# Kernel optimization log

Measured on AMD Instinct MI355X. Metric: run time of the kernel, lower is better.

The kernel has to match this reference:

```python
import jax, jax.numpy as jnp
import numpy as np

D_MODEL = 1024
NHEADS = 16
D_K = D_MODEL // NHEADS


def setup_inputs() -> dict:
    key = jax.random.key(0)
    ks = jax.random.split(key, 12)
    B, S = 2, 2048
    scale = 1.0 / np.sqrt(D_MODEL)
    inp = {
        "query": jax.random.normal(ks[0], (B, S, D_MODEL), dtype=jnp.float32),
        "key": jax.random.normal(ks[1], (B, S, D_MODEL), dtype=jnp.float32),
        "value": jax.random.normal(ks[2], (B, S, D_MODEL), dtype=jnp.float32),
        "mask": jax.random.randint(ks[3], (B, 1, S, S), 0, 2, dtype=jnp.int32),
        "Wq": jax.random.normal(ks[4], (D_MODEL, D_MODEL), dtype=jnp.float32) * scale,
        "bq": jnp.zeros((D_MODEL,), dtype=jnp.float32),
        "Wk": jax.random.normal(ks[5], (D_MODEL, D_MODEL), dtype=jnp.float32) * scale,
        "bk": jnp.zeros((D_MODEL,), dtype=jnp.float32),
        "Wv": jax.random.normal(ks[6], (D_MODEL, D_MODEL), dtype=jnp.float32) * scale,
        "bv": jnp.zeros((D_MODEL,), dtype=jnp.float32),
        "Wo": jax.random.normal(ks[7], (D_MODEL, D_MODEL), dtype=jnp.float32) * scale,
        "bo": jnp.zeros((D_MODEL,), dtype=jnp.float32),
    }
    return inp


def _split_heads(x):
    # [B, S, (H*D)] -> [B, H, S, D]
    B, S, _ = x.shape
    return x.reshape(B, S, NHEADS, D_K).transpose(0, 2, 1, 3)


def reference(query, key, value, mask, Wq, bq, Wk, bk, Wv, bv, Wo, bo):
    B, Sq, _ = query.shape
    q = _split_heads(query @ Wq + bq)            # [B, H, Sq, Dk]
    k = _split_heads(key @ Wk + bk)              # [B, H, Sk, Dk]
    v = _split_heads(value @ Wv + bv)            # [B, H, Sk, Dk]
    # scores: [B, H, Sq, Sk], scaled by sqrt(d_k)
    scores = jnp.einsum("bhqd,bhkd->bhqk", q, k) / np.sqrt(D_K).astype(np.float32)
    scores = jnp.where(mask == 0, jnp.float32(-1e12), scores)
    weights = jax.nn.softmax(scores, axis=-1)
    out = jnp.einsum("bhqk,bhkd->bhqd", weights, v)  # [B, H, Sq, Dk]
    out = out.transpose(0, 2, 1, 3).reshape(B, Sq, D_MODEL)
    return out @ Wo + bo  # dropout is identity in eval / p=0
```

## Files before the change

kernel.cpp:

```cpp
#include <hip/hip_runtime.h>
#include <math.h>

#define D_MODEL 1024
#define NHEADS  16
#define DK      64
#define BATCH   2
#define SEQ     2048
#define M_TOTAL (BATCH * SEQ)
#define NT      (SEQ / 64)
#define CK1 0.18033688011112042f
#define CK0 -17.312340490667561f

typedef __attribute__((ext_vector_type(8))) short bf16x8;
typedef __attribute__((ext_vector_type(4))) float f32x4;

__device__ __forceinline__ unsigned short f2bf(float f) {
    union { float f; unsigned int i; } v; v.f = f;
    return (unsigned short)((v.i + 0x7FFFu + ((v.i >> 16) & 1u)) >> 16);
}

__device__ __forceinline__ void async_copy16(const void* g, void* l) {
    __builtin_amdgcn_global_load_lds(
        (const __attribute__((address_space(1))) unsigned int*)g,
        (__attribute__((address_space(3))) unsigned int*)l, 16, 0, 0);
}

struct Cvt3 { const float* s[3]; unsigned short* d[3]; };
__global__ __launch_bounds__(256)
void cvt_flat(const Cvt3 a)
{
    const float* __restrict__ s = a.s[blockIdx.z];
    unsigned short* __restrict__ d = a.d[blockIdx.z];
    const size_t i = ((size_t)blockIdx.x * 256 + threadIdx.x) * 4;
    const float4 v = *reinterpret_cast<const float4*>(&s[i]);
    ushort4 o;
    o.x = f2bf(v.x); o.y = f2bf(v.y); o.z = f2bf(v.z); o.w = f2bf(v.w);
    *reinterpret_cast<ushort4*>(&d[i]) = o;
}

struct Cvt4 { const float* s[4]; unsigned short* d[4]; };
__global__ __launch_bounds__(256)
void cvt_wt(const Cvt4 a)
{
    __shared__ unsigned short t[32][33];
    const float* __restrict__ W = a.s[blockIdx.z];
    unsigned short* __restrict__ WT = a.d[blockIdx.z];
    const int tx = threadIdx.x & 31;
    const int ty = threadIdx.x >> 5;
    const int nb = blockIdx.x << 5;
    const int kb = blockIdx.y << 5;
#pragma unroll
    for (int i = 0; i < 4; ++i)
        t[ty + (i << 3)][tx] = f2bf(W[(size_t)(kb + ty + (i << 3)) * D_MODEL + nb + tx]);
    __syncthreads();
#pragma unroll
    for (int i = 0; i < 4; ++i)
        WT[(size_t)(nb + ty + (i << 3)) * D_MODEL + kb + tx] = t[tx][ty + (i << 3)];
}

__global__ __launch_bounds__(256)
void mask_pack(const int* __restrict__ mask, unsigned long long* __restrict__ wm)
{
    const int tid  = threadIdx.x;
    const int lane = tid & 63;
    const int l15  = lane & 15;
    const int kg   = lane >> 4;
    const int wv   = ((int)blockIdx.x << 2) + (tid >> 6);
    const int t    = wv & 31;
    const int qw   = (wv >> 5) & 127;
    const int bb   = wv >> 12;

    const int* mb = mask + (size_t)bb * SEQ * SEQ;
    const int qrow = (qw << 4) + (kg << 2);
    const int kcol = (t << 6) + l15;
    unsigned long long* wout = wm + ((((size_t)bb * 128 + qw) * 32 + t) << 4);

#pragma unroll
    for (int r = 0; r < 4; ++r)
#pragma unroll
        for (int n = 0; n < 4; ++n) {
            const int m = mb[(size_t)(qrow + r) * SEQ + kcol + (n << 4)];
            const unsigned long long bal = __ballot(m != 0);
            if (lane == 0) wout[(r << 2) | n] = bal;
        }
}

template <typename OutT> struct GArgs {
    const unsigned short* X[3];
    const unsigned short* W[3];
    const float*          Bi[3];
    OutT*                 O[3];
};

__device__ __forceinline__ void st_out(float* p, float v) { *p = v; }
__device__ __forceinline__ void st_out(unsigned short* p, float v) { *p = f2bf(v); }

template <typename OutT>
__global__ __launch_bounds__(256)
void gemm_bf16(const GArgs<OutT> args, const int head_split)
{
    __shared__ __align__(16) unsigned short As[128][32];
    __shared__ __align__(16) unsigned short Bs[128][32];

    const unsigned short* __restrict__ X  = args.X[blockIdx.z];
    const unsigned short* __restrict__ WT = args.W[blockIdx.z];
    const float* __restrict__ bias        = args.Bi[blockIdx.z];
    OutT* __restrict__ out                = args.O[blockIdx.z];

    const int tid = threadIdx.x;
    const int wid = tid >> 6;
    const int wy  = wid >> 1;
    const int wx  = wid & 1;
    const int l15 = tid & 15;
    const int kg  = (tid >> 4) & 3;

    const int id = ((int)blockIdx.y << 3) | (int)blockIdx.x;
    const int sw = ((id & 7) << 5) | (id >> 3);
    const int n0 = (sw & 7) << 7;
    const int m0 = (sw >> 3) << 7;

    const int lane = tid & 63;
    const int gr   = lane >> 2;
    const int gc   = (lane & 3) << 3;
    const int c0   = wid << 1;

    f32x4 acc[4][4];
#pragma unroll
    for (int i = 0; i < 4; ++i)
#pragma unroll
        for (int j = 0; j < 4; ++j)
            acc[i][j] = (f32x4){0.f, 0.f, 0.f, 0.f};

#pragma unroll 1
    for (int t = 0; t < D_MODEL / 32; ++t) {
        const int k0 = t << 5;

        __syncthreads();
#pragma unroll
        for (int cc = 0; cc < 2; ++cc) {
            const int c = c0 + cc;
            async_copy16(&X[(size_t)(m0 + (c << 4) + gr) * D_MODEL + k0 + gc],
                         &As[c << 4][0]);
            async_copy16(&WT[(size_t)(n0 + (c << 4) + gr) * D_MODEL + k0 + gc],
                         &Bs[c << 4][0]);
        }
        __syncthreads();

        bf16x8 a[4], b[4];
#pragma unroll
        for (int i = 0; i < 4; ++i)
            a[i] = *reinterpret_cast<const bf16x8*>(
                &As[(wy << 6) + (i << 4) + l15][kg << 3]);
#pragma unroll
        for (int j = 0; j < 4; ++j)
            b[j] = *reinterpret_cast<const bf16x8*>(
                &Bs[(wx << 6) + (j << 4) + l15][kg << 3]);
#pragma unroll
        for (int i = 0; i < 4; ++i)
#pragma unroll
            for (int j = 0; j < 4; ++j)
                acc[i][j] = __builtin_amdgcn_mfma_f32_16x16x32_bf16(
                    a[i], b[j], acc[i][j], 0, 0, 0);
    }

    float bv[4];
#pragma unroll
    for (int j = 0; j < 4; ++j)
        bv[j] = bias[n0 + (wx << 6) + (j << 4) + l15];

#pragma unroll
    for (int i = 0; i < 4; ++i) {
#pragma unroll
        for (int r = 0; r < 4; ++r) {
            const int m = m0 + (wy << 6) + (i << 4) + (kg << 2) + r;
#pragma unroll
            for (int j = 0; j < 4; ++j) {
                const int n = n0 + (wx << 6) + (j << 4) + l15;
                const float val = acc[i][j][r] + bv[j];
                if (head_split) {
                    const int bbx = m >> 11;
                    const int ss  = m & (SEQ - 1);
                    const int hhx = n >> 6;
                    const int dd  = n & (DK - 1);
                    st_out(&out[((size_t)(bbx * NHEADS + hhx) * SEQ + ss) * DK + dd], val);
                } else {
                    st_out(&out[(size_t)m * D_MODEL + n], val);
                }
            }
        }
    }
}

__global__ __launch_bounds__(256)
void flash_mfma(const unsigned short* __restrict__ Qb,
                const unsigned short* __restrict__ Kb,
                const unsigned short* __restrict__ Vb,
                const unsigned long long* __restrict__ wmask,
                unsigned short* __restrict__ ctx)
{
    __shared__ __align__(16) unsigned short Kbf[64][72];
    __shared__ __align__(16) unsigned short Vt [64][72];
    __shared__ __align__(16) unsigned short Pq [4][16][72];

    const int tid  = threadIdx.x;
    const int w    = tid >> 6;
    const int lane = tid & 63;
    const int l15  = lane & 15;
    const int kg   = lane >> 4;

    const int bb = blockIdx.z;
    const int hh = blockIdx.y;
    const int q0 = blockIdx.x << 6;

    const unsigned short* Qh = Qb + (size_t)(bb * NHEADS + hh) * SEQ * DK;
    const unsigned short* Kh = Kb + (size_t)(bb * NHEADS + hh) * SEQ * DK;
    const unsigned short* Vh = Vb + (size_t)(bb * NHEADS + hh) * SEQ * DK;

    bf16x8 aq[2];
    {
        const unsigned short* qrow = Qh + (size_t)(q0 + w * 16 + l15) * DK + (kg << 3);
        aq[0] = *reinterpret_cast<const bf16x8*>(qrow);
        aq[1] = *reinterpret_cast<const bf16x8*>(qrow + 32);
    }

    const int krow = tid >> 2;
    const int kcb  = (tid & 3) << 4;
    const int vkb  = (tid & 15) << 2;
    const int vdb  = (tid >> 4) << 2;

    const int wbase = __builtin_amdgcn_readfirstlane(
        (bb * 128 + (q0 >> 4) + w) << 9);

    float l_lane[4] = {0.f, 0.f, 0.f, 0.f};
    f32x4 O4[4];
#pragma unroll
    for (int n = 0; n < 4; ++n) O4[n] = (f32x4){0.f, 0.f, 0.f, 0.f};

    uint4 kv0 = *reinterpret_cast<const uint4*>(Kh + (size_t)krow * DK + kcb);
    uint4 kv1 = *reinterpret_cast<const uint4*>(Kh + (size_t)krow * DK + kcb + 8);
    uint2 vr[4];
#pragma unroll
    for (int i = 0; i < 4; ++i)
        vr[i] = *reinterpret_cast<const uint2*>(Vh + (size_t)(vkb + i) * DK + vdb);

#pragma unroll 1
    for (int t = 0; t < NT; ++t) {
        __syncthreads();
        *reinterpret_cast<uint4*>(&Kbf[krow][kcb])     = kv0;
        *reinterpret_cast<uint4*>(&Kbf[krow][kcb + 8]) = kv1;
        {
            uint2 o;
            o.x = (vr[0].x & 0xFFFFu) | (vr[1].x << 16);
            o.y = (vr[2].x & 0xFFFFu) | (vr[3].x << 16);
            *reinterpret_cast<uint2*>(&Vt[vdb + 0][vkb]) = o;
            o.x = (vr[0].x >> 16) | (vr[1].x & 0xFFFF0000u);
            o.y = (vr[2].x >> 16) | (vr[3].x & 0xFFFF0000u);
            *reinterpret_cast<uint2*>(&Vt[vdb + 1][vkb]) = o;
            o.x = (vr[0].y & 0xFFFFu) | (vr[1].y << 16);
            o.y = (vr[2].y & 0xFFFFu) | (vr[3].y << 16);
            *reinterpret_cast<uint2*>(&Vt[vdb + 2][vkb]) = o;
            o.x = (vr[0].y >> 16) | (vr[1].y & 0xFFFF0000u);
            o.y = (vr[2].y >> 16) | (vr[3].y & 0xFFFF0000u);
            *reinterpret_cast<uint2*>(&Vt[vdb + 3][vkb]) = o;
        }
        __syncthreads();

        if (t + 1 < NT) {
            const int kn = (t + 1) << 6;
            kv0 = *reinterpret_cast<const uint4*>(Kh + (size_t)(kn + krow) * DK + kcb);
            kv1 = *reinterpret_cast<const uint4*>(Kh + (size_t)(kn + krow) * DK + kcb + 8);
#pragma unroll
            for (int i = 0; i < 4; ++i)
                vr[i] = *reinterpret_cast<const uint2*>(
                    Vh + (size_t)(kn + vkb + i) * DK + vdb);
        }

        const unsigned long long* wmt = wmask + wbase + (t << 4);
        unsigned long long wmv[16];
#pragma unroll
        for (int rn = 0; rn < 16; ++rn) wmv[rn] = wmt[rn];

        f32x4 S[4];
#pragma unroll
        for (int n = 0; n < 4; ++n) {
            const bf16x8 b0 = *reinterpret_cast<const bf16x8*>(
                &Kbf[16 * n + l15][kg << 3]);
            const bf16x8 b1 = *reinterpret_cast<const bf16x8*>(
                &Kbf[16 * n + l15][(kg << 3) + 32]);
            f32x4 acc = (f32x4){0.f, 0.f, 0.f, 0.f};
            acc = __builtin_amdgcn_mfma_f32_16x16x32_bf16(aq[0], b0, acc, 0, 0, 0);
            acc = __builtin_amdgcn_mfma_f32_16x16x32_bf16(aq[1], b1, acc, 0, 0, 0);
            S[n] = acc;
        }

#pragma unroll
        for (int n = 0; n < 4; ++n)
#pragma unroll
            for (int r = 0; r < 4; ++r) {
                float x = fmaf(S[n][r], CK1, CK0);
                __asm__("v_exp_f32 %0, %1" : "=v"(x) : "v"(x));
                __asm__("v_cndmask_b32 %0, 0, %1, %2"
                        : "=v"(x) : "v"(x), "s"(wmv[(r << 2) | n]));
                l_lane[r] += x;
                unsigned pk;
                __asm__("v_cvt_pk_bf16_f32 %0, %1, %2"
                        : "=v"(pk) : "v"(x), "v"(x));
                Pq[w][(kg << 2) + r][16 * n + l15] = (unsigned short)pk;
            }

        __asm__ volatile("s_waitcnt lgkmcnt(0)" ::: "memory");

        const bf16x8 ap0 = *reinterpret_cast<const bf16x8*>(&Pq[w][l15][kg << 3]);
        const bf16x8 ap1 = *reinterpret_cast<const bf16x8*>(&Pq[w][l15][(kg << 3) + 32]);
#pragma unroll
        for (int n = 0; n < 4; ++n) {
            const bf16x8 b0 = *reinterpret_cast<const bf16x8*>(
                &Vt[16 * n + l15][kg << 3]);
            const bf16x8 b1 = *reinterpret_cast<const bf16x8*>(
                &Vt[16 * n + l15][(kg << 3) + 32]);
            O4[n] = __builtin_amdgcn_mfma_f32_16x16x32_bf16(ap0, b0, O4[n], 0, 0, 0);
            O4[n] = __builtin_amdgcn_mfma_f32_16x16x32_bf16(ap1, b1, O4[n], 0, 0, 0);
        }
    }

#pragma unroll
    for (int r = 0; r < 4; ++r) {
        float rsum = l_lane[r];
        rsum += __shfl_xor(rsum, 1);
        rsum += __shfl_xor(rsum, 2);
        rsum += __shfl_xor(rsum, 4);
        rsum += __shfl_xor(rsum, 8);
        const float inv = 1.f / rsum;
        const size_t base =
            (size_t)(bb * SEQ + q0 + w * 16 + (kg << 2) + r) * D_MODEL + hh * DK + l15;
#pragma unroll
        for (int n = 0; n < 4; ++n)
            ctx[base + 16 * n] = f2bf(O4[n][r] * inv);
    }
}

extern "C" void kernel_launch(void* const* d_in, const int* in_sizes, int n_in,
                              void* d_out, int out_size, void* d_ws, size_t ws_size,
                              hipStream_t stream)
{
    const float* query = (const float*)d_in[0];
    const float* key   = (const float*)d_in[1];
    const float* value = (const float*)d_in[2];
    const int*   mask  = (const int*)d_in[3];
    const float* Wq = (const float*)d_in[4];
    const float* bq = (const float*)d_in[5];
    const float* Wk = (const float*)d_in[6];
    const float* bk = (const float*)d_in[7];
    const float* Wv = (const float*)d_in[8];
    const float* bv = (const float*)d_in[9];
    const float* Wo = (const float*)d_in[10];
    const float* bo = (const float*)d_in[11];

    unsigned short* ws = (unsigned short*)d_ws;
    const size_t TE = (size_t)M_TOTAL * D_MODEL;
    const size_t WE = (size_t)D_MODEL * D_MODEL;
    unsigned short* Xq  = ws;
    unsigned short* Xk  = Xq + TE;
    unsigned short* Xv  = Xk + TE;
    unsigned short* WTq = Xv + TE;
    unsigned short* WTk = WTq + WE;
    unsigned short* WTv = WTk + WE;
    unsigned short* WTo = WTv + WE;
    unsigned short* Qb  = WTo + WE;
    unsigned short* Kb  = Qb + TE;
    unsigned short* Vb  = Kb + TE;
    unsigned short* Ctx = Vb + TE;
    unsigned long long* WM = (unsigned long long*)(Ctx + TE);

    Cvt3 c3;
    c3.s[0] = query; c3.s[1] = key; c3.s[2] = value;
    c3.d[0] = Xq;    c3.d[1] = Xk;  c3.d[2] = Xv;
    cvt_flat<<<dim3(TE / 1024, 1, 3), 256, 0, stream>>>(c3);

    Cvt4 c4;
    c4.s[0] = Wq;  c4.s[1] = Wk;  c4.s[2] = Wv;  c4.s[3] = Wo;
    c4.d[0] = WTq; c4.d[1] = WTk; c4.d[2] = WTv; c4.d[3] = WTo;
    cvt_wt<<<dim3(32, 32, 4), 256, 0, stream>>>(c4);

    mask_pack<<<dim3(2048, 1, 1), 256, 0, stream>>>(mask, WM);

    GArgs<unsigned short> qkv;
    qkv.X[0] = Xq;  qkv.X[1] = Xk;  qkv.X[2] = Xv;
    qkv.W[0] = WTq; qkv.W[1] = WTk; qkv.W[2] = WTv;
    qkv.Bi[0] = bq; qkv.Bi[1] = bk; qkv.Bi[2] = bv;
    qkv.O[0] = Qb;  qkv.O[1] = Kb;  qkv.O[2] = Vb;
    gemm_bf16<unsigned short><<<dim3(8, 32, 3), 256, 0, stream>>>(qkv, 1);

    flash_mfma<<<dim3(SEQ / 64, NHEADS, BATCH), 256, 0, stream>>>(
        Qb, Kb, Vb, WM, Ctx);

    GArgs<float> op;
    op.X[0] = Ctx;  op.X[1] = Ctx;  op.X[2] = Ctx;
    op.W[0] = WTo;  op.W[1] = WTo;  op.W[2] = WTo;
    op.Bi[0] = bo;  op.Bi[1] = bo;  op.Bi[2] = bo;
    op.O[0] = (float*)d_out; op.O[1] = (float*)d_out; op.O[2] = (float*)d_out;
    gemm_bf16<float><<<dim3(8, 32, 1), 256, 0, stream>>>(op, 0);
}
```

Baseline: 298.1 us.

## Keep softmax probabilities in registers via transposed QK MFMA and double-buffer K/V

The QK^T MFMA operands are swapped so each lane holds a score column in a layout that can be packed straight into the A operand of the PV MFMA. This removes the per-wave LDS round trip for P and its waitcnt. V is stored in LDS with a permuted k-order to match, K/V tiles are double-buffered so one barrier per iteration suffices, and block indices are swizzled to improve L2 locality. The mask packing kernel is also changed to vectorised int4 loads. The risk is correctness from the subtle k-order permutation of P and V and from row-sum reduction changes, plus extra LDS use.

```diff
diff --git a/kernel.cpp b/kernel.cpp
--- a/kernel.cpp
+++ b/kernel.cpp
@@ -70,17 +70,20 @@
     const int qw   = (wv >> 5) & 127;
     const int bb   = wv >> 12;
 
-    const int* mb = mask + (size_t)bb * SEQ * SEQ;
-    const int qrow = (qw << 4) + (kg << 2);
-    const int kcol = (t << 6) + l15;
+    const int* mb = mask + (size_t)bb * SEQ * SEQ
+                  + (size_t)((qw << 4) + l15) * SEQ + (t << 6) + (kg << 2);
     unsigned long long* wout = wm + ((((size_t)bb * 128 + qw) * 32 + t) << 4);
 
+    int4 ln[4];
+#pragma unroll
+    for (int n = 0; n < 4; ++n)
+        ln[n] = *reinterpret_cast<const int4*>(mb + (n << 4));
 #pragma unroll
     for (int r = 0; r < 4; ++r)
 #pragma unroll
         for (int n = 0; n < 4; ++n) {
-            const int m = mb[(size_t)(qrow + r) * SEQ + kcol + (n << 4)];
-            const unsigned long long bal = __ballot(m != 0);
+            const int mvv = (&ln[n].x)[r];
+            const unsigned long long bal = __ballot(mvv != 0);
             if (lane == 0) wout[(r << 2) | n] = bal;
         }
 }
@@ -198,9 +201,8 @@
                 const unsigned long long* __restrict__ wmask,
                 unsigned short* __restrict__ ctx)
 {
-    __shared__ __align__(16) unsigned short Kbf[64][72];
-    __shared__ __align__(16) unsigned short Vt [64][72];
-    __shared__ __align__(16) unsigned short Pq [4][16][72];
+    __shared__ __align__(16) unsigned short Kbf[2][64][72];
+    __shared__ __align__(16) unsigned short V3 [2][64][72];
 
     const int tid  = threadIdx.x;
     const int w    = tid >> 6;
@@ -208,9 +210,12 @@
     const int l15  = lane & 15;
     const int kg   = lane >> 4;
 
-    const int bb = blockIdx.z;
-    const int hh = blockIdx.y;
-    const int q0 = blockIdx.x << 6;
+    const int flat = ((int)blockIdx.z * NHEADS + (int)blockIdx.y) * (SEQ / 64)
+                   + (int)blockIdx.x;
+    const int swz  = ((flat & 7) << 7) | (flat >> 3);
+    const int q0 = (swz & 31) << 6;
+    const int hh = (swz >> 5) & 15;
+    const int bb = swz >> 9;
 
     const unsigned short* Qh = Qb + (size_t)(bb * NHEADS + hh) * SEQ * DK;
     const unsigned short* Kh = Kb + (size_t)(bb * NHEADS + hh) * SEQ * DK;
@@ -227,14 +232,15 @@
     const int kcb  = (tid & 3) << 4;
     const int vkb  = (tid & 15) << 2;
     const int vdb  = (tid >> 4) << 2;
+    const int voff = (((vkb >> 2) & 3) << 4) + ((vkb >> 4) << 2);
 
     const int wbase = __builtin_amdgcn_readfirstlane(
         (bb * 128 + (q0 >> 4) + w) << 9);
 
-    float l_lane[4] = {0.f, 0.f, 0.f, 0.f};
+    float lsum = 0.f;
     f32x4 O4[4];
 #pragma unroll
-    for (int n = 0; n < 4; ++n) O4[n] = (f32x4){0.f, 0.f, 0.f, 0.f};
+    for (int db = 0; db < 4; ++db) O4[db] = (f32x4){0.f, 0.f, 0.f, 0.f};
 
     uint4 kv0 = *reinterpret_cast<const uint4*>(Kh + (size_t)krow * DK + kcb);
     uint4 kv1 = *reinterpret_cast<const uint4*>(Kh + (size_t)krow * DK + kcb + 8);
@@ -245,23 +251,24 @@
 
 #pragma unroll 1
     for (int t = 0; t < NT; ++t) {
-        __syncthreads();
-        *reinterpret_cast<uint4*>(&Kbf[krow][kcb])     = kv0;
-        *reinterpret_cast<uint4*>(&Kbf[krow][kcb + 8]) = kv1;
+        const int c = t & 1;
+
+        *reinterpret_cast<uint4*>(&Kbf[c][krow][kcb])     = kv0;
+        *reinterpret_cast<uint4*>(&Kbf[c][krow][kcb + 8]) = kv1;
         {
             uint2 o;
             o.x = (vr[0].x & 0xFFFFu) | (vr[1].x << 16);
             o.y = (vr[2].x & 0xFFFFu) | (vr[3].x << 16);
-            *reinterpret_cast<uint2*>(&Vt[vdb + 0][vkb]) = o;
+            *reinterpret_cast<uint2*>(&V3[c][vdb + 0][voff]) = o;
             o.x = (vr[0].x >> 16) | (vr[1].x & 0xFFFF0000u);
             o.y = (vr[2].x >> 16) | (vr[3].x & 0xFFFF0000u);
-            *reinterpret_cast<uint2*>(&Vt[vdb + 1][vkb]) = o;
+            *reinterpret_cast<uint2*>(&V3[c][vdb + 1][voff]) = o;
             o.x = (vr[0].y & 0xFFFFu) | (vr[1].y << 16);
             o.y = (vr[2].y & 0xFFFFu) | (vr[3].y << 16);
-            *reinterpret_cast<uint2*>(&Vt[vdb + 2][vkb]) = o;
+            *reinterpret_cast<uint2*>(&V3[c][vdb + 2][voff]) = o;
             o.x = (vr[0].y >> 16) | (vr[1].y & 0xFFFF0000u);
             o.y = (vr[2].y >> 16) | (vr[3].y & 0xFFFF0000u);
-            *reinterpret_cast<uint2*>(&Vt[vdb + 3][vkb]) = o;
+            *reinterpret_cast<uint2*>(&V3[c][vdb + 3][voff]) = o;
         }
         __syncthreads();
 
@@ -284,58 +291,58 @@
 #pragma unroll
         for (int n = 0; n < 4; ++n) {
             const bf16x8 b0 = *reinterpret_cast<const bf16x8*>(
-                &Kbf[16 * n + l15][kg << 3]);
+                &Kbf[c][16 * n + l15][kg << 3]);
             const bf16x8 b1 = *reinterpret_cast<const bf16x8*>(
-                &Kbf[16 * n + l15][(kg << 3) + 32]);
+                &Kbf[c][16 * n + l15][(kg << 3) + 32]);
             f32x4 acc = (f32x4){0.f, 0.f, 0.f, 0.f};
-            acc = __builtin_amdgcn_mfma_f32_16x16x32_bf16(aq[0], b0, acc, 0, 0, 0);
-            acc = __builtin_amdgcn_mfma_f32_16x16x32_bf16(aq[1], b1, acc, 0, 0, 0);
+            acc = __builtin_amdgcn_mfma_f32_16x16x32_bf16(b0, aq[0], acc, 0, 0, 0);
+            acc = __builtin_amdgcn_mfma_f32_16x16x32_bf16(b1, aq[1], acc, 0, 0, 0);
             S[n] = acc;
         }
 
-#pragma unroll
-        for (int n = 0; n < 4; ++n)
+        unsigned pw01[4], pw23[4];
+#pragma unroll
+        for (int n = 0; n < 4; ++n) {
+            float xv[4];
 #pragma unroll
             for (int r = 0; r < 4; ++r) {
-                float x = fmaf(S[n][r], CK1, CK0);
-                __asm__("v_exp_f32 %0, %1" : "=v"(x) : "v"(x));
+                float e = fmaf(S[n][r], CK1, CK0);
+                __asm__("v_exp_f32 %0, %1" : "=v"(e) : "v"(e));
                 __asm__("v_cndmask_b32 %0, 0, %1, %2"
-                        : "=v"(x) : "v"(x), "s"(wmv[(r << 2) | n]));
-                l_lane[r] += x;
-                unsigned pk;
-                __asm__("v_cvt_pk_bf16_f32 %0, %1, %2"
-                        : "=v"(pk) : "v"(x), "v"(x));
-                Pq[w][(kg << 2) + r][16 * n + l15] = (unsigned short)pk;
+                        : "=v"(e) : "v"(e), "s"(wmv[(r << 2) | n]));
+                lsum += e;
+                xv[r] = e;
             }
-
-        __asm__ volatile("s_waitcnt lgkmcnt(0)" ::: "memory");
-
-        const bf16x8 ap0 = *reinterpret_cast<const bf16x8*>(&Pq[w][l15][kg << 3]);
-        const bf16x8 ap1 = *reinterpret_cast<const bf16x8*>(&Pq[w][l15][(kg << 3) + 32]);
-#pragma unroll
-        for (int n = 0; n < 4; ++n) {
-            const bf16x8 b0 = *reinterpret_cast<const bf16x8*>(
-                &Vt[16 * n + l15][kg << 3]);
-            const bf16x8 b1 = *reinterpret_cast<const bf16x8*>(
-                &Vt[16 * n + l15][(kg << 3) + 32]);
-            O4[n] = __builtin_amdgcn_mfma_f32_16x16x32_bf16(ap0, b0, O4[n], 0, 0, 0);
-            O4[n] = __builtin_amdgcn_mfma_f32_16x16x32_bf16(ap1, b1, O4[n], 0, 0, 0);
+            __asm__("v_cvt_pk_bf16_f32 %0, %1, %2"
+                    : "=v"(pw01[n]) : "v"(xv[0]), "v"(xv[1]));
+            __asm__("v_cvt_pk_bf16_f32 %0, %1, %2"
+                    : "=v"(pw23[n]) : "v"(xv[2]), "v"(xv[3]));
+        }
+        union { unsigned u[4]; bf16x8 v; } pa0, pa1;
+        pa0.u[0] = pw01[0]; pa0.u[1] = pw23[0]; pa0.u[2] = pw01[1]; pa0.u[3] = pw23[1];
+        pa1.u[0] = pw01[2]; pa1.u[1] = pw23[2]; pa1.u[2] = pw01[3]; pa1.u[3] = pw23[3];
+
+#pragma unroll
+        for (int db = 0; db < 4; ++db) {
+            const unsigned short* vbase = &V3[c][(db << 4) + l15][kg << 4];
+            const bf16x8 v0 = *reinterpret_cast<const bf16x8*>(vbase);
+            const bf16x8 v1 = *reinterpret_cast<const bf16x8*>(vbase + 8);
+            O4[db] = __builtin_amdgcn_mfma_f32_16x16x32_bf16(pa0.v, v0, O4[db], 0, 0, 0);
+            O4[db] = __builtin_amdgcn_mfma_f32_16x16x32_bf16(pa1.v, v1, O4[db], 0, 0, 0);
         }
     }
 
+    lsum += __shfl_xor(lsum, 16);
+    lsum += __shfl_xor(lsum, 32);
 #pragma unroll
     for (int r = 0; r < 4; ++r) {
-        float rsum = l_lane[r];
-        rsum += __shfl_xor(rsum, 1);
-        rsum += __shfl_xor(rsum, 2);
-        rsum += __shfl_xor(rsum, 4);
-        rsum += __shfl_xor(rsum, 8);
-        const float inv = 1.f / rsum;
+        const float rs = __shfl(lsum, (kg << 2) + r);
+        const float inv = 1.f / rs;
         const size_t base =
             (size_t)(bb * SEQ + q0 + w * 16 + (kg << 2) + r) * D_MODEL + hh * DK + l15;
 #pragma unroll
-        for (int n = 0; n < 4; ++n)
-            ctx[base + 16 * n] = f2bf(O4[n][r] * inv);
+        for (int db = 0; db < 4; ++db)
+            ctx[base + 16 * db] = f2bf(O4[db][r] * inv);
     }
 }
 
```

Result: faster. 290.6 us (-2.5%).
